# Optimization experiments

Measured on AMD Instinct MI355X. Metric: run time of the kernel, lower is better.

The kernel has to match this reference:

```python
import jax, jax.numpy as jnp
import numpy as np

D_MODEL = 2048
NUM_EXPERTS = 64
TOP_K = 2


def setup_inputs() -> dict:
    key = jax.random.key(0)
    kx, kw, kb = jax.random.split(key, 3)
    x = jax.random.normal(kx, (4, 4096, D_MODEL), dtype=jnp.float32)
    # nn.Linear(d_model, num_experts): weight [num_experts, d_model], bias [num_experts]
    bound = 1.0 / np.sqrt(D_MODEL)
    W = jax.random.uniform(kw, (NUM_EXPERTS, D_MODEL), minval=-bound, maxval=bound, dtype=jnp.float32)
    b = jax.random.uniform(kb, (NUM_EXPERTS,), minval=-bound, maxval=bound, dtype=jnp.float32)
    return {"x": x, "W": W, "b": b}


def reference(x, W, b):
    # Eval mode: no noise injection (self.training is False).
    logits = jnp.einsum('bsd,ed->bse', x, W) + b          # [B, S, E]
    raw_weights = jax.nn.softmax(logits, axis=-1)          # [B, S, E]
    top_k_weights, top_k_indices = jax.lax.top_k(raw_weights, TOP_K)  # [B, S, K]
    normalized = top_k_weights / jnp.sum(top_k_weights, axis=-1, keepdims=True)
    return normalized, top_k_indices
```

## Files before the change

kernel.cpp:

```cpp
#include <hip/hip_runtime.h>
#include <math.h>

#define DM 2048
#define NEXP 64
#define NTOK 16384
#define KC 32
#define KSL 512
#define NCH (KSL / KC)
#define MBLK 32
#define NBLK (NTOK / MBLK)
#define NKG (DM / KC)
#define WFRAG_BYTES (NKG * 12 * 1024)
#define QS 2120

typedef __attribute__((ext_vector_type(8))) short short8;
typedef __attribute__((ext_vector_type(4))) short short4v;
typedef __attribute__((ext_vector_type(4))) float f32x4;

__device__ __forceinline__ void split3t(float f, unsigned short& h,
                                        unsigned short& m, unsigned short& l) {
  unsigned u = __float_as_uint(f);
  h = (unsigned short)(u >> 16);
  float f1 = f - __uint_as_float(u & 0xFFFF0000u);
  unsigned u1 = __float_as_uint(f1);
  m = (unsigned short)(u1 >> 16);
  float f2 = f1 - __uint_as_float(u1 & 0xFFFF0000u);
  l = (unsigned short)(__float_as_uint(f2) >> 16);
}

__device__ __forceinline__ void split8(const f32x4& a0, const f32x4& a1,
                                       short8& h, short8& m, short8& l) {
  float v[8] = {a0[0], a0[1], a0[2], a0[3], a1[0], a1[1], a1[2], a1[3]};
#pragma unroll
  for (int j = 0; j < 8; ++j) {
    unsigned short hh, mm, ll;
    split3t(v[j], hh, mm, ll);
    h[j] = (short)hh; m[j] = (short)mm; l[j] = (short)ll;
  }
}

__global__ void convw_kernel(const float* __restrict__ W,
                             unsigned short* __restrict__ wfrag) {
  const int kg = blockIdx.x;
  const int lane = threadIdx.x & 63;
  const int nt = threadIdx.x >> 6;
  const int e = nt * 16 + (lane & 15);
  const int kpos = kg * 32 + (lane >> 4) * 8;
  const f32x4* wp = (const f32x4*)(W + (size_t)e * DM + kpos);
  f32x4 w0 = wp[0], w1 = wp[1];
  short8 h, m, l;
  split8(w0, w1, h, m, l);
  size_t base = ((size_t)(kg * 12 + nt) * 64 + lane) * 8;
  *(short8*)(wfrag + base) = h;
  *(short8*)(wfrag + base + (size_t)4 * 64 * 8) = m;
  *(short8*)(wfrag + base + (size_t)8 * 64 * 8) = l;
}

__global__ __launch_bounds__(256, 4)
void router_fused(const float* __restrict__ x,
                  const unsigned short* __restrict__ wfrag,
                  const float* __restrict__ bias, float* __restrict__ out) {
  const int lane = threadIdx.x & 63;
  const int wv = threadIdx.x >> 6;
  const int col = lane & 15;
  const int quad = lane >> 4;
  const int tok0 = blockIdx.x * MBLK;
  const int kg0 = wv * NCH;

  __shared__ float pl[4 * QS];

  const float* xp0 = x + (size_t)(tok0 + col) * DM + wv * KSL + quad * 8;
  const float* xp1 = xp0 + (size_t)16 * DM;
  const unsigned short* bb = wfrag + (size_t)lane * 8;

  f32x4 acc[2][4];
#pragma unroll
  for (int mt = 0; mt < 2; ++mt)
#pragma unroll
    for (int nt = 0; nt < 4; ++nt) acc[mt][nt] = (f32x4){0.f, 0.f, 0.f, 0.f};

  f32x4 P00 = ((const f32x4*)xp0)[0], P01 = ((const f32x4*)xp0)[1];
  f32x4 P10 = ((const f32x4*)xp1)[0], P11 = ((const f32x4*)xp1)[1];
  f32x4 Q00 = ((const f32x4*)(xp0 + KC))[0], Q01 = ((const f32x4*)(xp0 + KC))[1];
  f32x4 Q10 = ((const f32x4*)(xp1 + KC))[0], Q11 = ((const f32x4*)(xp1 + KC))[1];

#pragma unroll 2
  for (int c = 0; c < NCH; ++c) {
    const int kg = kg0 + c;
    short8 ah0, am0, al0, ah1, am1, al1;
    split8(P00, P01, ah0, am0, al0);
    split8(P10, P11, ah1, am1, al1);
    P00 = Q00; P01 = Q01; P10 = Q10; P11 = Q11;
    if (c + 2 < NCH) {
      const float* n0 = xp0 + (size_t)(c + 2) * KC;
      const float* n1 = xp1 + (size_t)(c + 2) * KC;
      Q00 = ((const f32x4*)n0)[0]; Q01 = ((const f32x4*)n0)[1];
      Q10 = ((const f32x4*)n1)[0]; Q11 = ((const f32x4*)n1)[1];
    }
#pragma unroll
    for (int nt = 0; nt < 4; ++nt) {
      const int g = kg * 12 + nt;
      short8 bh = *(const short8*)(bb + (size_t)(g + 0) * 512);
      short8 bm = *(const short8*)(bb + (size_t)(g + 4) * 512);
      short8 bl = *(const short8*)(bb + (size_t)(g + 8) * 512);
      {
        f32x4 cc = acc[0][nt];
        cc = __builtin_amdgcn_mfma_f32_16x16x32_bf16(ah0, bh, cc, 0, 0, 0);
        cc = __builtin_amdgcn_mfma_f32_16x16x32_bf16(ah0, bm, cc, 0, 0, 0);
        cc = __builtin_amdgcn_mfma_f32_16x16x32_bf16(am0, bh, cc, 0, 0, 0);
        cc = __builtin_amdgcn_mfma_f32_16x16x32_bf16(ah0, bl, cc, 0, 0, 0);
        cc = __builtin_amdgcn_mfma_f32_16x16x32_bf16(al0, bh, cc, 0, 0, 0);
        cc = __builtin_amdgcn_mfma_f32_16x16x32_bf16(am0, bm, cc, 0, 0, 0);
        acc[0][nt] = cc;
      }
      {
        f32x4 cc = acc[1][nt];
        cc = __builtin_amdgcn_mfma_f32_16x16x32_bf16(ah1, bh, cc, 0, 0, 0);
        cc = __builtin_amdgcn_mfma_f32_16x16x32_bf16(ah1, bm, cc, 0, 0, 0);
        cc = __builtin_amdgcn_mfma_f32_16x16x32_bf16(am1, bh, cc, 0, 0, 0);
        cc = __builtin_amdgcn_mfma_f32_16x16x32_bf16(ah1, bl, cc, 0, 0, 0);
        cc = __builtin_amdgcn_mfma_f32_16x16x32_bf16(al1, bh, cc, 0, 0, 0);
        cc = __builtin_amdgcn_mfma_f32_16x16x32_bf16(am1, bm, cc, 0, 0, 0);
        acc[1][nt] = cc;
      }
    }
  }

#pragma unroll
  for (int mt = 0; mt < 2; ++mt)
#pragma unroll
    for (int nt = 0; nt < 4; ++nt)
#pragma unroll
      for (int r = 0; r < 4; ++r)
        pl[wv * QS + (mt * 16 + quad * 4 + r) * 66 + nt * 16 + col] =
            acc[mt][nt][r];
  __syncthreads();

  if (wv < 2) {
    const int tt = lane & 15;
    const int q = lane >> 4;
    const int tl = wv * 16 + tt;
    float v1 = -INFINITY, v2 = -INFINITY;
    int i1 = 0, i2 = 0;
#pragma unroll
    for (int e = 0; e < NEXP; ++e) {
      float p = pl[q * QS + tl * 66 + e];
      p += __shfl_xor(p, 16, 64);
      p += __shfl_xor(p, 32, 64);
      const float v = p + bias[e];
      const bool a = v > v1;
      const bool b = v > v2;
      const float nv2 = a ? v1 : (b ? v : v2);
      const int ni2 = a ? i1 : (b ? e : i2);
      v2 = nv2; i2 = ni2;
      i1 = a ? e : i1;
      v1 = a ? v : v1;
    }
    if (q == 0) {
      const int t = tok0 + tl;
      const float ex = expf(v2 - v1);
      const float den = 1.f + ex;
      *(float2*)(out + 2 * t) = make_float2(1.f / den, ex / den);
      *(float2*)(out + 2 * NTOK + 2 * t) = make_float2((float)i1, (float)i2);
    }
  }
}

__global__ __launch_bounds__(512, 2)
void router_fb(const float* __restrict__ x, const float* __restrict__ W,
               const float* __restrict__ bias, float* __restrict__ out) {
  const int lane = threadIdx.x & 63;
  const int wv = threadIdx.x >> 6;
  const int col = lane & 15;
  const int quad = lane >> 4;
  const int tok0 = blockIdx.x * 32;
  const int k0 = wv * 256;

  __shared__ float part[8][32][68];

  f32x4 acc[2][4];
#pragma unroll
  for (int ms = 0; ms < 2; ++ms)
#pragma unroll
    for (int nt = 0; nt < 4; ++nt) acc[ms][nt] = (f32x4){0.f, 0.f, 0.f, 0.f};

  for (int ks = 0; ks < 8; ++ks) {
    const int k = k0 + ks * 32 + quad * 8;
    short8 ah[2], am2[2], al2[2];
#pragma unroll
    for (int ms = 0; ms < 2; ++ms) {
      const f32x4* ap = (const f32x4*)(x + (size_t)(tok0 + ms * 16 + col) * DM + k);
      f32x4 a0 = ap[0], a1 = ap[1];
      split8(a0, a1, ah[ms], am2[ms], al2[ms]);
    }
#pragma unroll
    for (int nt = 0; nt < 4; ++nt) {
      short8 bh, bm, bl;
      const f32x4* wp = (const f32x4*)(W + (size_t)(nt * 16 + col) * DM + k);
      f32x4 w0 = wp[0], w1 = wp[1];
      split8(w0, w1, bh, bm, bl);
#pragma unroll
      for (int ms = 0; ms < 2; ++ms) {
        f32x4 cc = acc[ms][nt];
        cc = __builtin_amdgcn_mfma_f32_16x16x32_bf16(ah[ms], bh, cc, 0, 0, 0);
        cc = __builtin_amdgcn_mfma_f32_16x16x32_bf16(ah[ms], bm, cc, 0, 0, 0);
        cc = __builtin_amdgcn_mfma_f32_16x16x32_bf16(am2[ms], bh, cc, 0, 0, 0);
        cc = __builtin_amdgcn_mfma_f32_16x16x32_bf16(ah[ms], bl, cc, 0, 0, 0);
        cc = __builtin_amdgcn_mfma_f32_16x16x32_bf16(al2[ms], bh, cc, 0, 0, 0);
        cc = __builtin_amdgcn_mfma_f32_16x16x32_bf16(am2[ms], bm, cc, 0, 0, 0);
        acc[ms][nt] = cc;
      }
    }
  }
#pragma unroll
  for (int ms = 0; ms < 2; ++ms)
#pragma unroll
    for (int nt = 0; nt < 4; ++nt)
#pragma unroll
      for (int r = 0; r < 4; ++r)
        part[wv][ms * 16 + quad * 4 + r][nt * 16 + col] = acc[ms][nt][r];
  __syncthreads();
  const float bl_ = bias[lane];
#pragma unroll
  for (int ti = 0; ti < 4; ++ti) {
    const int t = wv * 4 + ti;
    float v1 = bl_;
#pragma unroll
    for (int p = 0; p < 8; ++p) v1 += part[p][t][lane];
    int i1 = lane;
    float v2 = -INFINITY;
    int i2 = NEXP;
#pragma unroll
    for (int off = 32; off > 0; off >>= 1) {
      float ov1 = __shfl_xor(v1, off, 64);
      int   oi1 = __shfl_xor(i1, off, 64);
      float ov2 = __shfl_xor(v2, off, 64);
      int   oi2 = __shfl_xor(i2, off, 64);
      bool afirst = (v1 > ov1) || (v1 == ov1 && i1 < oi1);
      float w1v = afirst ? v1 : ov1;  int w1i = afirst ? i1 : oi1;
      float c1v = afirst ? v2 : ov2;  int c1i = afirst ? i2 : oi2;
      float c2v = afirst ? ov1 : v1;  int c2i = afirst ? oi1 : i1;
      bool sfirst = (c1v > c2v) || (c1v == c2v && c1i < c2i);
      v1 = w1v; i1 = w1i;
      v2 = sfirst ? c1v : c2v;
      i2 = sfirst ? c1i : c2i;
    }
    if (lane == 0) {
      const float ex = expf(v2 - v1);
      const float den = 1.f + ex;
      const int token = tok0 + t;
      *(float2*)(out + 2 * token) = make_float2(1.f / den, ex / den);
      *(float2*)(out + 2 * NTOK + 2 * token) =
          make_float2((float)i1, (float)i2);
    }
  }
}

extern "C" void kernel_launch(void* const* d_in, const int* in_sizes, int n_in,
                              void* d_out, int out_size, void* d_ws, size_t ws_size,
                              hipStream_t stream) {
  const float* x = (const float*)d_in[0];
  const float* W = (const float*)d_in[1];
  const float* b = (const float*)d_in[2];
  float* out = (float*)d_out;

  const size_t need = (size_t)WFRAG_BYTES + 16384;
  if (ws_size >= need) {
    unsigned short* wfrag = (unsigned short*)d_ws;
    hipLaunchKernelGGL(convw_kernel, dim3(NKG), dim3(256), 0, stream, W, wfrag);
    hipLaunchKernelGGL(router_fused, dim3(NBLK), dim3(256), 0, stream,
                       x, wfrag, b, out);
  } else {
    hipLaunchKernelGGL(router_fb, dim3(NTOK / 32), dim3(512), 0, stream,
                       x, W, b, out);
  }
}
```

Before: 210.8 us.

## Split GEMM K across two blocks and add separate top-2 reduce kernel

Each token group's K dimension is now split across two blocks (doubling the grid to 1024 blocks), each writing partial logits to a global workspace. A new reduce kernel sums the two halves, adds bias, and does top-2 selection and softmax normalization. This is meant to raise parallelism and occupancy over the 512-block grid. In exchange it adds an extra launch and an 8 MB round trip through global memory for the partial logits, and it needs a larger workspace, otherwise the fallback path runs.

```diff
diff --git a/kernel.cpp b/kernel.cpp
--- a/kernel.cpp
+++ b/kernel.cpp
@@ -5,12 +5,12 @@
 #define NEXP 64
 #define NTOK 16384
 #define KC 32
-#define KSL 512
-#define NCH (KSL / KC)
+#define NCHW 8
 #define MBLK 32
-#define NBLK (NTOK / MBLK)
+#define NBLK (2 * NTOK / MBLK)
 #define NKG (DM / KC)
 #define WFRAG_BYTES (NKG * 12 * 1024)
+#define PART_BYTES (2 * NEXP * NTOK * 4)
 #define QS 2120
 
 typedef __attribute__((ext_vector_type(8))) short short8;
@@ -57,19 +57,21 @@
 }
 
 __global__ __launch_bounds__(256, 4)
-void router_fused(const float* __restrict__ x,
-                  const unsigned short* __restrict__ wfrag,
-                  const float* __restrict__ bias, float* __restrict__ out) {
+void router_gemm(const float* __restrict__ x,
+                 const unsigned short* __restrict__ wfrag,
+                 float* __restrict__ part) {
   const int lane = threadIdx.x & 63;
   const int wv = threadIdx.x >> 6;
   const int col = lane & 15;
   const int quad = lane >> 4;
-  const int tok0 = blockIdx.x * MBLK;
-  const int kg0 = wv * NCH;
+  const int tg = blockIdx.x >> 1;
+  const int half = blockIdx.x & 1;
+  const int tok0 = tg * MBLK;
+  const int kg0 = (half * 4 + wv) * NCHW;
 
   __shared__ float pl[4 * QS];
 
-  const float* xp0 = x + (size_t)(tok0 + col) * DM + wv * KSL + quad * 8;
+  const float* xp0 = x + (size_t)(tok0 + col) * DM + kg0 * KC + quad * 8;
   const float* xp1 = xp0 + (size_t)16 * DM;
   const unsigned short* bb = wfrag + (size_t)lane * 8;
 
@@ -85,13 +87,13 @@
   f32x4 Q10 = ((const f32x4*)(xp1 + KC))[0], Q11 = ((const f32x4*)(xp1 + KC))[1];
 
 #pragma unroll 2
-  for (int c = 0; c < NCH; ++c) {
+  for (int c = 0; c < NCHW; ++c) {
     const int kg = kg0 + c;
     short8 ah0, am0, al0, ah1, am1, al1;
     split8(P00, P01, ah0, am0, al0);
     split8(P10, P11, ah1, am1, al1);
     P00 = Q00; P01 = Q01; P10 = Q10; P11 = Q11;
-    if (c + 2 < NCH) {
+    if (c + 2 < NCHW) {
       const float* n0 = xp0 + (size_t)(c + 2) * KC;
       const float* n1 = xp1 + (size_t)(c + 2) * KC;
       Q00 = ((const f32x4*)n0)[0]; Q01 = ((const f32x4*)n0)[1];
@@ -136,34 +138,42 @@
             acc[mt][nt][r];
   __syncthreads();
 
-  if (wv < 2) {
-    const int tt = lane & 15;
-    const int q = lane >> 4;
-    const int tl = wv * 16 + tt;
-    float v1 = -INFINITY, v2 = -INFINITY;
-    int i1 = 0, i2 = 0;
-#pragma unroll
-    for (int e = 0; e < NEXP; ++e) {
-      float p = pl[q * QS + tl * 66 + e];
-      p += __shfl_xor(p, 16, 64);
-      p += __shfl_xor(p, 32, 64);
-      const float v = p + bias[e];
-      const bool a = v > v1;
-      const bool b = v > v2;
-      const float nv2 = a ? v1 : (b ? v : v2);
-      const int ni2 = a ? i1 : (b ? e : i2);
-      v2 = nv2; i2 = ni2;
-      i1 = a ? e : i1;
-      v1 = a ? v : v1;
-    }
-    if (q == 0) {
-      const int t = tok0 + tl;
-      const float ex = expf(v2 - v1);
-      const float den = 1.f + ex;
-      *(float2*)(out + 2 * t) = make_float2(1.f / den, ex / den);
-      *(float2*)(out + 2 * NTOK + 2 * t) = make_float2((float)i1, (float)i2);
-    }
-  }
+  {
+    const int t = threadIdx.x & 31;
+    const int e8 = threadIdx.x >> 5;
+#pragma unroll
+    for (int i = 0; i < 8; ++i) {
+      const int e = e8 * 8 + i;
+      float v = pl[0 * QS + t * 66 + e] + pl[1 * QS + t * 66 + e] +
+                pl[2 * QS + t * 66 + e] + pl[3 * QS + t * 66 + e];
+      part[(size_t)(half * NEXP + e) * NTOK + tok0 + t] = v;
+    }
+  }
+}
+
+__global__ __launch_bounds__(128, 8)
+void router_reduce(const float* __restrict__ part,
+                   const float* __restrict__ bias, float* __restrict__ out) {
+  const int t = blockIdx.x * 128 + threadIdx.x;
+
+  float v1 = -INFINITY, v2 = -INFINITY;
+  int i1 = 0, i2 = 0;
+#pragma unroll
+  for (int e = 0; e < NEXP; ++e) {
+    const float v = part[(size_t)e * NTOK + t] +
+                    part[(size_t)(NEXP + e) * NTOK + t] + bias[e];
+    const bool a = v > v1;
+    const bool b = v > v2;
+    const float nv2 = a ? v1 : (b ? v : v2);
+    const int ni2 = a ? i1 : (b ? e : i2);
+    v2 = nv2; i2 = ni2;
+    i1 = a ? e : i1;
+    v1 = a ? v : v1;
+  }
+  const float ex = expf(v2 - v1);
+  const float den = 1.f + ex;
+  *(float2*)(out + 2 * t) = make_float2(1.f / den, ex / den);
+  *(float2*)(out + 2 * NTOK + 2 * t) = make_float2((float)i1, (float)i2);
 }
 
 __global__ __launch_bounds__(512, 2)
@@ -264,12 +274,15 @@
   const float* b = (const float*)d_in[2];
   float* out = (float*)d_out;
 
-  const size_t need = (size_t)WFRAG_BYTES + 16384;
+  const size_t need = (size_t)WFRAG_BYTES + (size_t)PART_BYTES;
   if (ws_size >= need) {
     unsigned short* wfrag = (unsigned short*)d_ws;
+    float* part = (float*)((char*)d_ws + WFRAG_BYTES);
     hipLaunchKernelGGL(convw_kernel, dim3(NKG), dim3(256), 0, stream, W, wfrag);
-    hipLaunchKernelGGL(router_fused, dim3(NBLK), dim3(256), 0, stream,
-                       x, wfrag, b, out);
+    hipLaunchKernelGGL(router_gemm, dim3(NBLK), dim3(256), 0, stream,
+                       x, wfrag, part);
+    hipLaunchKernelGGL(router_reduce, dim3(NTOK / 128), dim3(128), 0, stream,
+                       part, b, out);
   } else {
     hipLaunchKernelGGL(router_fb, dim3(NTOK / 32), dim3(512), 0, stream,
                        x, W, b, out);
```

Measured after the change: 217.7 us. 1.03x slower.
